# Kernel tuning notes

Hardware: AMD Instinct MI355X
Metric: run time of the kernel (lower is better)

The kernel has to match this reference:

```python
import jax, jax.numpy as jnp
import numpy as np

HIDDEN = 2048
NH = 32        # query heads
NKV = 4        # kv heads (GQA)
HD = 64        # head_dim
Q_SIZE = NH * HD      # 2048
KV_SIZE = NKV * HD    # 256
WINDOW = 1024         # sliding window size
THETA = 1000000.0
T = 2048              # tokens
SCALE = HD ** -0.5
NEG = -1e30


def setup_inputs() -> dict:
    key = jax.random.key(0)
    k1, k2, k3 = jax.random.split(key, 3)
    return {
        "positions": jnp.arange(T, dtype=jnp.int32),
        "hidden_states": jax.random.normal(k1, (T, HIDDEN), dtype=jnp.float32),
        "wqkv": jax.random.normal(k2, (HIDDEN, Q_SIZE + 2 * KV_SIZE), dtype=jnp.float32) * (HIDDEN ** -0.5),
        "wo": jax.random.normal(k3, (Q_SIZE, HIDDEN), dtype=jnp.float32) * (Q_SIZE ** -0.5),
    }


def _apply_rope(x, positions):
    # NeoX-style rotary embedding over full head_dim (rotate halves).
    half = HD // 2
    inv_freq = 1.0 / (THETA ** (jnp.arange(half, dtype=jnp.float32) / half))
    ang = positions.astype(jnp.float32)[:, None] * inv_freq[None, :]   # [T, half]
    cos = jnp.cos(ang)[:, None, :]   # [T, 1, half]
    sin = jnp.sin(ang)[:, None, :]
    x1, x2 = jnp.split(x, 2, axis=-1)
    return jnp.concatenate([x1 * cos - x2 * sin, x2 * cos + x1 * sin], axis=-1)


def reference(positions, hidden_states, wqkv, wo):
    # fused QKV projection
    qkv = hidden_states @ wqkv                          # [T, Q+2KV]
    q = qkv[:, :Q_SIZE].reshape(T, NH, HD)
    k = qkv[:, Q_SIZE:Q_SIZE + KV_SIZE].reshape(T, NKV, HD)
    v = qkv[:, Q_SIZE + KV_SIZE:].reshape(T, NKV, HD)
    # rotary embedding on q, k
    q = _apply_rope(q, positions)
    k = _apply_rope(k, positions)
    # GQA: repeat kv heads to match query heads
    group = NH // NKV
    kr = jnp.repeat(k, group, axis=1)                   # [T, NH, HD]
    vr = jnp.repeat(v, group, axis=1)
    scores = jnp.einsum('qhd,khd->hqk', q, kr) * SCALE  # [NH, T, T]
    # causal + sliding-window mask: attend to j in (i-WINDOW, i]
    i = jnp.arange(T)[:, None]
    j = jnp.arange(T)[None, :]
    mask = (j <= i) & (i - j < WINDOW)                  # [T, T]
    scores = jnp.where(mask[None, :, :], scores, NEG)
    probs = jax.nn.softmax(scores, axis=-1)
    attn = jnp.einsum('hqk,khd->qhd', probs, vr).reshape(T, Q_SIZE)
    return attn @ wo                                    # [T, HIDDEN]
```

## Files before the change

### kernel.cpp

```cpp
#include <hip/hip_runtime.h>
#include <hip/hip_bf16.h>

typedef float  f32x4  __attribute__((ext_vector_type(4)));
typedef __bf16 bf16x8 __attribute__((ext_vector_type(8)));
typedef __bf16 bf16x4 __attribute__((ext_vector_type(4)));
typedef __bf16 bf16x2 __attribute__((ext_vector_type(2)));

#define T_SEQ   2048
#define HIDDEN  2048
#define NH      32
#define NKV     4
#define HD      64
#define QSZ     2048
#define KVSZ    256
#define QKVN    2560
#define WINDOW  1024
#define QSCALE  0.1803368801111f

__device__ __forceinline__ void gll16(const __bf16* g, __bf16* l) {
    __builtin_amdgcn_global_load_lds(
        (const __attribute__((address_space(1))) void*)g,
        (__attribute__((address_space(3))) void*)l,
        16, 0, 0);
}

__global__ __launch_bounds__(256) void cvt_f32_bf16(const float4* __restrict__ in,
                                                    bf16x4* __restrict__ out) {
    int id = blockIdx.x * 256 + threadIdx.x;
    float4 v = in[id];
    bf16x4 o;
    o[0] = (__bf16)v.x; o[1] = (__bf16)v.y; o[2] = (__bf16)v.z; o[3] = (__bf16)v.w;
    out[id] = o;
}

__global__ __launch_bounds__(256) void transpose_f32_bf16(const float* __restrict__ in,
                                                          __bf16* __restrict__ out,
                                                          int Rin, int Cin) {
    __shared__ float tile[32][33];
    int r = threadIdx.x >> 5;
    int c = threadIdx.x & 31;
    int ri = blockIdx.y * 32, ci = blockIdx.x * 32;
    #pragma unroll
    for (int i = 0; i < 4; i++)
        tile[r + i*8][c] = in[(size_t)(ri + r + i*8) * Cin + ci + c];
    __syncthreads();
    #pragma unroll
    for (int i = 0; i < 4; i++)
        out[(size_t)(ci + r + i*8) * Rin + ri + c] = (__bf16)tile[c][r + i*8];
}


#define GEMM_PROLOGUE(Aptr, Btptr, Kdim)                                        \
    __shared__ __align__(16) __bf16 Asm[2][64 * 64];                            \
    __shared__ __align__(16) __bf16 Bsm[2][128 * 64];                           \
    const int tid = threadIdx.x;                                                \
    const int wid = tid >> 6;                                                   \
    const int l   = tid & 63;                                                   \
    const int lg  = l >> 4;                                                     \
    const int ll  = l & 15;                                                     \
    const int swl = ll & 7;                                                     \
    const int wm  = wid >> 1, wn = wid & 1;                                     \
    const int gx   = gridDim.x;                                                 \
    const int flat = blockIdx.y * gx + blockIdx.x;                              \
    const int nwg  = gx * gridDim.y;                                            \
    const int swz  = (flat & 7) * (nwg >> 3) + (flat >> 3);                     \
    const int bm   = (swz / gx) * 64;                                           \
    const int bn   = (swz % gx) * 128;                                          \
    const __bf16* Ab = (Aptr) + (size_t)bm * (Kdim);                            \
    const __bf16* Bb = (Btptr) + (size_t)bn * (Kdim);                           \
    f32x4 acc[2][4];                                                            \
    _Pragma("unroll")                                                           \
    for (int i = 0; i < 2; i++)                                                 \
        _Pragma("unroll")                                                       \
        for (int j = 0; j < 4; j++)                                             \
            acc[i][j] = (f32x4){0.f, 0.f, 0.f, 0.f};                            \
    const int srow = tid >> 3;                                                  \
    const int sseg0 = tid & 7;

#define GEMM_STAGE(buf, k0, Kdim)                                               \
    {                                                                           \
        _Pragma("unroll")                                                       \
        for (int c = 0; c < 2; c++) {                                           \
            int row  = c * 32 + srow;                                           \
            int sseg = sseg0 ^ (row & 7);                                       \
            gll16(Ab + (size_t)row * (Kdim) + (k0) + sseg * 8,                  \
                  &Asm[buf][(c * 256 + tid) * 8]);                              \
        }                                                                       \
        _Pragma("unroll")                                                       \
        for (int c = 0; c < 4; c++) {                                           \
            int row  = c * 32 + srow;                                           \
            int sseg = sseg0 ^ (row & 7);                                       \
            gll16(Bb + (size_t)row * (Kdim) + (k0) + sseg * 8,                  \
                  &Bsm[buf][(c * 256 + tid) * 8]);                              \
        }                                                                       \
    }

#define GEMM_KLOOP(Kdim)                                                        \
    GEMM_STAGE(0, 0, Kdim)                                                      \
    __syncthreads();                                                            \
    int cur = 0;                                                                \
    for (int k0 = 0; k0 < (Kdim); k0 += 64) {                                   \
        if (k0 + 64 < (Kdim)) GEMM_STAGE(cur ^ 1, k0 + 64, Kdim)                \
        _Pragma("unroll")                                                       \
        for (int ss = 0; ss < 2; ss++) {                                        \
            bf16x8 af[2], bfr[4];                                               \
            _Pragma("unroll")                                                   \
            for (int mi = 0; mi < 2; mi++) {                                    \
                int r = wm * 32 + mi * 16 + ll;                                 \
                int u = (ss * 4 + lg) ^ swl;                                    \
                af[mi] = *reinterpret_cast<const bf16x8*>(&Asm[cur][r * 64 + u * 8]); \
            }                                                                   \
            _Pragma("unroll")                                                   \
            for (int ni = 0; ni < 4; ni++) {                                    \
                int r = wn * 64 + ni * 16 + ll;                                 \
                int u = (ss * 4 + lg) ^ swl;                                    \
                bfr[ni] = *reinterpret_cast<const bf16x8*>(&Bsm[cur][r * 64 + u * 8]); \
            }                                                                   \
            _Pragma("unroll")                                                   \
            for (int mi = 0; mi < 2; mi++)                                      \
                _Pragma("unroll")                                               \
                for (int ni = 0; ni < 4; ni++)                                  \
                    acc[mi][ni] = __builtin_amdgcn_mfma_f32_16x16x32_bf16(      \
                        af[mi], bfr[ni], acc[mi][ni], 0, 0, 0);                 \
        }                                                                       \
        __syncthreads();                                                        \
        cur ^= 1;                                                               \
    }

__global__ __launch_bounds__(256) void gemm_out(const __bf16* __restrict__ A,
                                                const __bf16* __restrict__ Bt,
                                                float* __restrict__ Cout,
                                                int M, int N, int K) {
    GEMM_PROLOGUE(A, Bt, K)
    GEMM_KLOOP(K)
    #pragma unroll
    for (int mi = 0; mi < 2; mi++)
        #pragma unroll
        for (int ni = 0; ni < 4; ni++)
            #pragma unroll
            for (int r = 0; r < 4; r++) {
                int row = bm + wm*32 + mi*16 + lg*4 + r;
                int col = bn + wn*64 + ni*16 + ll;
                Cout[(size_t)row * N + col] = acc[mi][ni][r];
            }
}

__global__ __launch_bounds__(256) void gemm_qkv(const __bf16* __restrict__ A,
                                                const __bf16* __restrict__ Bt,
                                                const int* __restrict__ pos,
                                                __bf16* __restrict__ q,
                                                __bf16* __restrict__ k,
                                                __bf16* __restrict__ vT) {
    GEMM_PROLOGUE(A, Bt, HIDDEN)
    GEMM_KLOOP(HIDDEN)

    if (bn < QSZ + KVSZ) {
        const bool isq = (bn < QSZ);
        const float ifr0 = exp2f((float)ll * -0.62286151779138f);
        const float ifr1 = exp2f((float)(16 + ll) * -0.62286151779138f);
        #pragma unroll
        for (int mi = 0; mi < 2; mi++) {
            #pragma unroll
            for (int r = 0; r < 4; r++) {
                int row = bm + wm*32 + mi*16 + lg*4 + r;
                float p = (float)pos[row];
                #pragma unroll
                for (int ni = 0; ni < 2; ni++) {
                    float ang = p * (ni ? ifr1 : ifr0);
                    float sn, cs;
                    sincosf(ang, &sn, &cs);
                    float x1 = acc[mi][ni][r], x2 = acc[mi][ni + 2][r];
                    float o1 = x1 * cs - x2 * sn;
                    float o2 = x2 * cs + x1 * sn;
                    int col = bn + wn*64 + ni*16 + ll;
                    if (isq) {
                        q[(size_t)row * QSZ + col]      = (__bf16)(o1 * QSCALE);
                        q[(size_t)row * QSZ + col + 32] = (__bf16)(o2 * QSCALE);
                    } else {
                        k[(size_t)row * KVSZ + (col - QSZ)]      = (__bf16)o1;
                        k[(size_t)row * KVSZ + (col - QSZ) + 32] = (__bf16)o2;
                    }
                }
            }
        }
    } else {
        #pragma unroll
        for (int mi = 0; mi < 2; mi++) {
            int row0 = bm + wm*32 + mi*16 + lg*4;
            #pragma unroll
            for (int ni = 0; ni < 4; ni++) {
                int d = bn + wn*64 + ni*16 + ll - (QSZ + KVSZ);
                bf16x4 pk;
                #pragma unroll
                for (int r = 0; r < 4; r++) pk[r] = (__bf16)acc[mi][ni][r];
                *reinterpret_cast<bf16x4*>(&vT[(size_t)d * T_SEQ + row0]) = pk;
            }
        }
    }
}

__global__ __launch_bounds__(512) void attn_kernel(const __bf16* __restrict__ qg,
                                                   const __bf16* __restrict__ kgl,
                                                   const __bf16* __restrict__ vTg,
                                                   __bf16* __restrict__ og) {
    const int qb  = blockIdx.x;
    const int hp  = blockIdx.y;
    const int kvh = hp >> 2;
    const int tid = threadIdx.x;
    const int wid = tid >> 6;
    const int h   = hp * 2 + (wid >> 2);
    const int l   = tid & 63;
    const int lg  = l >> 4;
    const int ll  = l & 15;
    const int i0  = qb * 64;
    const int qw  = i0 + (wid & 3) * 16;
    const int qi  = qw + ll;

    __shared__ __align__(16) __bf16 Ksm[2][64 * 64];
    __shared__ __align__(16) __bf16 VTs[2][64 * 64];
    __shared__ __align__(16) __bf16 Psm[8][16][72];

    bf16x8 qf[2];
    {
        const __bf16* qp = qg + (size_t)(qw + ll) * QSZ + h * 64 + lg * 8;
        qf[0] = *reinterpret_cast<const bf16x8*>(qp);
        qf[1] = *reinterpret_cast<const bf16x8*>(qp + 32);
    }

    f32x4 o[4];
    #pragma unroll
    for (int dn = 0; dn < 4; dn++) o[dn] = (f32x4){0.f, 0.f, 0.f, 0.f};
    float l_run = 0.f;

    int jlo = i0 - (WINDOW - 1); if (jlo < 0) jlo = 0;
    int t0v = jlo & ~63;
    int tend = i0 + 64;

    const int srow = tid >> 3;
    const int sg   = (tid & 7) ^ (srow & 7);
    const __bf16* kp = kgl + (size_t)srow * KVSZ + kvh * 64 + sg * 8;
    const __bf16* vp = vTg + (size_t)(kvh * 64 + srow) * T_SEQ + sg * 8;

#define ASTAGE(buf, t)                                   \
    {                                                    \
        gll16(kp + (size_t)(t) * KVSZ, &Ksm[buf][tid * 8]); \
        gll16(vp + (t),                &VTs[buf][tid * 8]); \
    }

    ASTAGE(0, t0v);
    __syncthreads();

    const int swl = ll & 7;
    const int u0 = (lg ^ swl) * 8;
    const int u1 = ((4 + lg) ^ swl) * 8;

    int cur = 0;
    for (int t = t0v; t < tend; t += 64) {
        if (t + 64 < tend) ASTAGE(cur ^ 1, t + 64);

        bool active = (t <= qw + 15) && (t + 63 >= qw - (WINDOW - 1));
        if (active) {
            f32x4 sT[4];
            __builtin_amdgcn_s_setprio(1);
            #pragma unroll
            for (int kt = 0; kt < 4; kt++) {
                sT[kt] = (f32x4){0.f, 0.f, 0.f, 0.f};
                bf16x8 kf0 = *reinterpret_cast<const bf16x8*>(&Ksm[cur][kt*1024 + ll*64 + u0]);
                sT[kt] = __builtin_amdgcn_mfma_f32_16x16x32_bf16(kf0, qf[0], sT[kt], 0, 0, 0);
                bf16x8 kf1 = *reinterpret_cast<const bf16x8*>(&Ksm[cur][kt*1024 + ll*64 + u1]);
                sT[kt] = __builtin_amdgcn_mfma_f32_16x16x32_bf16(kf1, qf[1], sT[kt], 0, 0, 0);
            }
            __builtin_amdgcn_s_setprio(0);

            bool full = (t + 63 <= qw) && (t >= qw + 15 - (WINDOW - 1));
            float ts = 0.f;
            #pragma unroll
            for (int kt = 0; kt < 4; kt++) {
                float p0, p1, p2, p3;
                if (full) {
                    p0 = exp2f(sT[kt][0]);
                    p1 = exp2f(sT[kt][1]);
                    p2 = exp2f(sT[kt][2]);
                    p3 = exp2f(sT[kt][3]);
                } else {
                    int j = t + kt * 16 + lg * 4;
                    bool ok0 = (j     <= qi) && (qi - j     < WINDOW);
                    bool ok1 = (j + 1 <= qi) && (qi - j - 1 < WINDOW);
                    bool ok2 = (j + 2 <= qi) && (qi - j - 2 < WINDOW);
                    bool ok3 = (j + 3 <= qi) && (qi - j - 3 < WINDOW);
                    p0 = ok0 ? exp2f(sT[kt][0]) : 0.f;
                    p1 = ok1 ? exp2f(sT[kt][1]) : 0.f;
                    p2 = ok2 ? exp2f(sT[kt][2]) : 0.f;
                    p3 = ok3 ? exp2f(sT[kt][3]) : 0.f;
                }
                ts += (p0 + p1) + (p2 + p3);
                *reinterpret_cast<bf16x2*>(&Psm[wid][ll][kt*16 + lg*4])     = (bf16x2){(__bf16)p0, (__bf16)p1};
                *reinterpret_cast<bf16x2*>(&Psm[wid][ll][kt*16 + lg*4 + 2]) = (bf16x2){(__bf16)p2, (__bf16)p3};
            }
            ts += __shfl_xor(ts, 16);
            ts += __shfl_xor(ts, 32);
            l_run += ts;

            __builtin_amdgcn_s_setprio(1);
            #pragma unroll
            for (int kt2 = 0; kt2 < 2; kt2++) {
                bf16x8 pa = *reinterpret_cast<const bf16x8*>(&Psm[wid][ll][kt2*32 + lg*8]);
                int uv = kt2 ? u1 : u0;
                #pragma unroll
                for (int dn = 0; dn < 4; dn++) {
                    bf16x8 vf = *reinterpret_cast<const bf16x8*>(&VTs[cur][dn*1024 + ll*64 + uv]);
                    o[dn] = __builtin_amdgcn_mfma_f32_16x16x32_bf16(pa, vf, o[dn], 0, 0, 0);
                }
            }
            __builtin_amdgcn_s_setprio(0);
        }
        __syncthreads();
        cur ^= 1;
    }
#undef ASTAGE

    float linv = 1.0f / l_run;
    float i0v = __shfl(linv, lg*4 + 0);
    float i1v = __shfl(linv, lg*4 + 1);
    float i2v = __shfl(linv, lg*4 + 2);
    float i3v = __shfl(linv, lg*4 + 3);
    #pragma unroll
    for (int dn = 0; dn < 4; dn++) {
        og[(size_t)(qw + lg*4 + 0) * QSZ + h*64 + dn*16 + ll] = (__bf16)(o[dn][0] * i0v);
        og[(size_t)(qw + lg*4 + 1) * QSZ + h*64 + dn*16 + ll] = (__bf16)(o[dn][1] * i1v);
        og[(size_t)(qw + lg*4 + 2) * QSZ + h*64 + dn*16 + ll] = (__bf16)(o[dn][2] * i2v);
        og[(size_t)(qw + lg*4 + 3) * QSZ + h*64 + dn*16 + ll] = (__bf16)(o[dn][3] * i3v);
    }
}

extern "C" void kernel_launch(void* const* d_in, const int* in_sizes, int n_in,
                              void* d_out, int out_size, void* d_ws, size_t ws_size,
                              hipStream_t stream) {
    const int*   positions = (const int*)d_in[0];
    const float* hidden    = (const float*)d_in[1];
    const float* wqkv      = (const float*)d_in[2];
    const float* wo        = (const float*)d_in[3];
    float* out = (float*)d_out;

    char* ws = (char*)d_ws;
    __bf16* hidden_bf = (__bf16*)(ws);
    __bf16* wqkv_t    = (__bf16*)(ws + 8388608);
    __bf16* wo_t      = (__bf16*)(ws + 18874368);
    __bf16* q_bf      = (__bf16*)(ws + 37748736);
    __bf16* k_bf      = (__bf16*)(ws + 46137344);
    __bf16* vT_bf     = (__bf16*)(ws + 47185920);
    __bf16* attn_bf   = (__bf16*)(ws + 48234496);

    cvt_f32_bf16<<<dim3((T_SEQ * HIDDEN) / 4 / 256), dim3(256), 0, stream>>>(
        (const float4*)hidden, (bf16x4*)hidden_bf);
    transpose_f32_bf16<<<dim3(QKVN / 32, HIDDEN / 32), dim3(256), 0, stream>>>(
        wqkv, wqkv_t, HIDDEN, QKVN);
    transpose_f32_bf16<<<dim3(HIDDEN / 32, QSZ / 32), dim3(256), 0, stream>>>(
        wo, wo_t, QSZ, HIDDEN);

    gemm_qkv<<<dim3(QKVN / 128, T_SEQ / 64), dim3(256), 0, stream>>>(
        hidden_bf, wqkv_t, positions, q_bf, k_bf, vT_bf);

    attn_kernel<<<dim3(T_SEQ / 64, 16), dim3(512), 0, stream>>>(
        q_bf, k_bf, vT_bf, attn_bf);

    gemm_out<<<dim3(HIDDEN / 128, T_SEQ / 64), dim3(256), 0, stream>>>(
        attn_bf, wo_t, out, T_SEQ, HIDDEN, QSZ);
}
```

Measured before the change: 122.6 us.

## Keep attention probabilities in registers by permuting K rows, dropping LDS P staging

Permutes the K rows loaded into shared memory so the score MFMA output layout matches the A-operand layout of the PV MFMA. Probabilities are then packed straight from registers into bf16 fragments, which removes the per-wave Psm shared buffer and its LDS write/read round trip. The mask column index is recomputed to follow the new permutation. The exp is switched to the raw hardware exp2 builtin when it is available, with a fallback that changes the scale constant.

Result: faster. 113.4 us (-7.5%).

```diff
diff --git a/kernel.cpp b/kernel.cpp
--- a/kernel.cpp
+++ b/kernel.cpp
@@ -15,7 +15,14 @@
 #define KVSZ    256
 #define QKVN    2560
 #define WINDOW  1024
+
+#if __has_builtin(__builtin_amdgcn_exp2f)
+#define EXPS(x) __builtin_amdgcn_exp2f(x)
 #define QSCALE  0.1803368801111f
+#else
+#define EXPS(x) __expf(x)
+#define QSCALE  0.125f
+#endif
 
 __device__ __forceinline__ void gll16(const __bf16* g, __bf16* l) {
     __builtin_amdgcn_global_load_lds(
@@ -218,7 +225,6 @@
 
     __shared__ __align__(16) __bf16 Ksm[2][64 * 64];
     __shared__ __align__(16) __bf16 VTs[2][64 * 64];
-    __shared__ __align__(16) __bf16 Psm[8][16][72];
 
     bf16x8 qf[2];
     {
@@ -238,11 +244,12 @@
 
     const int srow = tid >> 3;
     const int sg   = (tid & 7) ^ (srow & 7);
-    const __bf16* kp = kgl + (size_t)srow * KVSZ + kvh * 64 + sg * 8;
+    const int krow = (srow & 35) | ((srow & 8) << 1) | ((srow & 4) << 1) | ((srow & 16) >> 2);
+    const __bf16* kp = kgl + (size_t)krow * KVSZ + kvh * 64 + sg * 8;
     const __bf16* vp = vTg + (size_t)(kvh * 64 + srow) * T_SEQ + sg * 8;
 
-#define ASTAGE(buf, t)                                   \
-    {                                                    \
+#define ASTAGE(buf, t)                                      \
+    {                                                       \
         gll16(kp + (size_t)(t) * KVSZ, &Ksm[buf][tid * 8]); \
         gll16(vp + (t),                &VTs[buf][tid * 8]); \
     }
@@ -274,28 +281,29 @@
 
             bool full = (t + 63 <= qw) && (t >= qw + 15 - (WINDOW - 1));
             float ts = 0.f;
-            #pragma unroll
-            for (int kt = 0; kt < 4; kt++) {
-                float p0, p1, p2, p3;
-                if (full) {
-                    p0 = exp2f(sT[kt][0]);
-                    p1 = exp2f(sT[kt][1]);
-                    p2 = exp2f(sT[kt][2]);
-                    p3 = exp2f(sT[kt][3]);
-                } else {
-                    int j = t + kt * 16 + lg * 4;
-                    bool ok0 = (j     <= qi) && (qi - j     < WINDOW);
-                    bool ok1 = (j + 1 <= qi) && (qi - j - 1 < WINDOW);
-                    bool ok2 = (j + 2 <= qi) && (qi - j - 2 < WINDOW);
-                    bool ok3 = (j + 3 <= qi) && (qi - j - 3 < WINDOW);
-                    p0 = ok0 ? exp2f(sT[kt][0]) : 0.f;
-                    p1 = ok1 ? exp2f(sT[kt][1]) : 0.f;
-                    p2 = ok2 ? exp2f(sT[kt][2]) : 0.f;
-                    p3 = ok3 ? exp2f(sT[kt][3]) : 0.f;
-                }
-                ts += (p0 + p1) + (p2 + p3);
-                *reinterpret_cast<bf16x2*>(&Psm[wid][ll][kt*16 + lg*4])     = (bf16x2){(__bf16)p0, (__bf16)p1};
-                *reinterpret_cast<bf16x2*>(&Psm[wid][ll][kt*16 + lg*4 + 2]) = (bf16x2){(__bf16)p2, (__bf16)p3};
+            if (full) {
+                #pragma unroll
+                for (int kt = 0; kt < 4; kt++) {
+                    #pragma unroll
+                    for (int r = 0; r < 4; r++) {
+                        float p = EXPS(sT[kt][r]);
+                        sT[kt][r] = p;
+                        ts += p;
+                    }
+                }
+            } else {
+                #pragma unroll
+                for (int kt = 0; kt < 4; kt++) {
+                    int jb = t + ((kt & 2) << 4) + ((kt & 1) << 2) + (lg << 3);
+                    #pragma unroll
+                    for (int r = 0; r < 4; r++) {
+                        int j = jb + r;
+                        bool ok = (j <= qi) && (qi - j < WINDOW);
+                        float p = ok ? EXPS(sT[kt][r]) : 0.f;
+                        sT[kt][r] = p;
+                        ts += p;
+                    }
+                }
             }
             ts += __shfl_xor(ts, 16);
             ts += __shfl_xor(ts, 32);
@@ -304,7 +312,12 @@
             __builtin_amdgcn_s_setprio(1);
             #pragma unroll
             for (int kt2 = 0; kt2 < 2; kt2++) {
-                bf16x8 pa = *reinterpret_cast<const bf16x8*>(&Psm[wid][ll][kt2*32 + lg*8]);
+                bf16x8 pa;
+                #pragma unroll
+                for (int r = 0; r < 4; r++) {
+                    pa[r]     = (__bf16)sT[kt2*2][r];
+                    pa[r + 4] = (__bf16)sT[kt2*2 + 1][r];
+                }
                 int uv = kt2 ? u1 : u0;
                 #pragma unroll
                 for (int dn = 0; dn < 4; dn++) {
```
